# Kernel tuning notes

Hardware: AMD Instinct MI355X
Metric: run time of the kernel (lower is better)

Reference implementation:

```python
import jax, jax.numpy as jnp
import numpy as np
import math

B, S, D, H, HD, P = 2, 2048, 2048, 16, 128, 10
ROPE_BASE = 10000.0


def _rope_tables(seq_len, head_dim):
    inv_freq = 1.0 / (ROPE_BASE ** (np.arange(0, head_dim, 2, dtype=np.float32) / head_dim))
    t = np.arange(seq_len, dtype=np.float32)
    freqs = np.outer(t, inv_freq)                  # [S, hd/2]
    emb = np.concatenate([freqs, freqs], axis=-1)  # [S, hd]
    return jnp.asarray(np.cos(emb)), jnp.asarray(np.sin(emb))


def _rotate_half(x):
    half = x.shape[-1] // 2
    return jnp.concatenate([-x[..., half:], x[..., :half]], axis=-1)


def setup_inputs() -> dict:
    key = jax.random.key(0)
    ks = jax.random.split(key, 8)
    hidden_states = jax.random.normal(ks[0], (B, S, D), dtype=jnp.float32)
    # causal additive mask, llama convention: 0 where allowed, large negative above diagonal
    causal = jnp.triu(jnp.full((S, S), -1e9, dtype=jnp.float32), k=1)
    attention_mask = jnp.broadcast_to(causal[None, None], (B, 1, S, S))
    position_ids = jnp.broadcast_to(jnp.arange(S, dtype=jnp.int64)[None], (B, S))
    scale = 1.0 / math.sqrt(D)
    Wq = jax.random.normal(ks[1], (D, D), dtype=jnp.float32) * scale
    Wk = jax.random.normal(ks[2], (D, D), dtype=jnp.float32) * scale
    Wv = jax.random.normal(ks[3], (D, D), dtype=jnp.float32) * scale
    Wo = jax.random.normal(ks[4], (D, D), dtype=jnp.float32) * scale
    adapter_query = jax.random.normal(ks[5], (P, D), dtype=jnp.float32)
    adapter_gate = jax.random.normal(ks[6], (1, H, 1, 1), dtype=jnp.float32) * 0.1
    return dict(hidden_states=hidden_states, attention_mask=attention_mask,
                position_ids=position_ids, Wq=Wq, Wk=Wk, Wv=Wv, Wo=Wo,
                adapter_query=adapter_query, adapter_gate=adapter_gate)


def reference(hidden_states, attention_mask, position_ids, Wq, Wk, Wv, Wo,
              adapter_query, adapter_gate):
    bsz, q_len, _ = hidden_states.shape
    inv_sqrt_hd = 1.0 / math.sqrt(HD)

    def split_heads(x):  # [B,S,D] -> [B,H,S,hd]
        return x.reshape(bsz, q_len, H, HD).transpose(0, 2, 1, 3)

    q = split_heads(hidden_states @ Wq)
    k = split_heads(hidden_states @ Wk)
    v = split_heads(hidden_states @ Wv)

    # RoPE
    cos_t, sin_t = _rope_tables(q_len, HD)
    cos = cos_t[position_ids][:, None]  # [B,1,S,hd]
    sin = sin_t[position_ids][:, None]
    q = q * cos + _rotate_half(q) * sin
    k = k * cos + _rotate_half(k) * sin

    # main attention
    scores = jnp.einsum('bhqd,bhkd->bhqk', q, k) * inv_sqrt_hd
    scores = scores + attention_mask
    attn = jax.nn.softmax(scores.astype(jnp.float32), axis=-1).astype(q.dtype)
    attn_out = jnp.einsum('bhqk,bhkd->bhqd', attn, v)

    # adapter: soft prompt projected through k/v proj (learn_kv=False), no RoPE
    adapter = jnp.broadcast_to(adapter_query[None], (bsz, P, D))  # [B,P,D]
    a_k = (adapter @ Wk).reshape(bsz, P, H, HD).transpose(0, 2, 1, 3)  # [B,H,P,hd]
    a_v = (adapter @ Wv).reshape(bsz, P, H, HD).transpose(0, 2, 1, 3)
    a_scores = jnp.einsum('bhqd,bhpd->bhqp', q, a_k) * inv_sqrt_hd
    a_w = adapter_gate * jax.nn.softmax(a_scores.astype(jnp.float32), axis=-1).astype(q.dtype)
    a_out = jnp.einsum('bhqp,bhpd->bhqd', a_w, a_v)

    out = attn_out + a_out
    out = out.transpose(0, 2, 1, 3).reshape(bsz, q_len, D)
    return out @ Wo
```

## Files before the change

### kernel.cpp

```cpp
#include <hip/hip_runtime.h>
#include <cstdint>
#include <cstddef>

typedef __bf16 bf16x8 __attribute__((ext_vector_type(8)));
typedef float  f32x4  __attribute__((ext_vector_type(4)));

__device__ __forceinline__ unsigned short f2bf(float f) {
  unsigned int u = __float_as_uint(f);
  u += 0x7FFF + ((u >> 16) & 1);
  return (unsigned short)(u >> 16);
}
__device__ __forceinline__ float bf2f(unsigned short u) {
  return __uint_as_float(((unsigned int)u) << 16);
}

#define SEQ 2048
#define DMODEL 2048
#define NH 16
#define HD 128
#define NB 2
#define NP 10
#define MAUG 4106
#define SCALEL2 (0.08838834764831845f * 1.44269504088896340f)

#define GLOAD_LDS16(g, l) \
  __builtin_amdgcn_global_load_lds((__attribute__((address_space(1))) const void*)(g), \
                                   (__attribute__((address_space(3))) void*)(l), 16, 0, 0)

#define FENCE() asm volatile("" ::: "memory")
#define SBAR() do { FENCE(); __builtin_amdgcn_s_barrier(); FENCE(); } while (0)
#define WAITVM(N) asm volatile("s_waitcnt vmcnt(" #N ")" ::: "memory")

__global__ void k_tables(float* __restrict__ cost, float* __restrict__ sint) {
  int idx = blockIdx.x * 256 + threadIdx.x;
  if (idx >= SEQ * 64) return;
  int s = idx >> 6, i = idx & 63;
  double invf = exp(-((double)(2 * i) / 128.0) * log(10000.0));
  double a = (double)s * invf;
  float c = (float)cos(a), sn = (float)sin(a);
  cost[s * HD + i] = c;  cost[s * HD + 64 + i] = c;
  sint[s * HD + i] = sn; sint[s * HD + 64 + i] = sn;
}

__global__ __launch_bounds__(256) void k_wt(const float* __restrict__ W0,
                                            const float* __restrict__ W1,
                                            const float* __restrict__ W2,
                                            const float* __restrict__ W3,
                                            unsigned short* __restrict__ out) {
  __shared__ float tile[32][33];
  const float* W = (blockIdx.z == 0) ? W0 : (blockIdx.z == 1) ? W1 : (blockIdx.z == 2) ? W2 : W3;
  unsigned short* o = out + (size_t)blockIdx.z * DMODEL * DMODEL;
  int bx = blockIdx.x * 32, by = blockIdx.y * 32;
  int tx = threadIdx.x & 31, ty = threadIdx.x >> 5;
  #pragma unroll
  for (int j = 0; j < 32; j += 8)
    tile[ty + j][tx] = W[(size_t)(bx + ty + j) * DMODEL + by + tx];
  __syncthreads();
  #pragma unroll
  for (int j = 0; j < 32; j += 8)
    o[(size_t)(by + ty + j) * DMODEL + bx + tx] = f2bf(tile[tx][ty + j]);
}

__global__ void k_xaug(const float* __restrict__ X, const float* __restrict__ Aq,
                       unsigned short* __restrict__ xaug) {
  size_t idx = (size_t)blockIdx.x * 256 + threadIdx.x;
  if (idx >= (size_t)MAUG * DMODEL) return;
  size_t row = idx >> 11;
  int col = (int)(idx & 2047);
  float v = (row < (size_t)NB * SEQ) ? X[idx] : Aq[(row - NB * SEQ) * DMODEL + col];
  xaug[idx] = f2bf(v);
}

#define RD_A(dst, bb, MH) do { \
  _Pragma("unroll") for (int i_ = 0; i_ < 4; i_++) \
    _Pragma("unroll") for (int ks_ = 0; ks_ < 2; ks_++) \
      dst[i_][ks_] = *(const bf16x8*)&lds[(bb) + (wr*128 + (MH)*64 + i_*16 + lr)*64 + (((ks_*4+quad) ^ (lr & 7)) * 8)]; \
} while (0)

#define RD_B(dst, bb, NHH) do { \
  _Pragma("unroll") for (int j_ = 0; j_ < 2; j_++) \
    _Pragma("unroll") for (int ks_ = 0; ks_ < 2; ks_++) \
      dst[j_][ks_] = *(const bf16x8*)&lds[(bb) + 16384 + (wc*64 + (NHH)*32 + j_*16 + lr)*64 + (((ks_*4+quad) ^ (lr & 7)) * 8)]; \
} while (0)

#define MM(A, B, MH, NHH) do { \
  __builtin_amdgcn_s_setprio(1); \
  _Pragma("unroll") for (int i_ = 0; i_ < 4; i_++) \
    _Pragma("unroll") for (int j_ = 0; j_ < 2; j_++) { \
      acc[(MH)*4+i_][(NHH)*2+j_] = __builtin_amdgcn_mfma_f32_16x16x32_bf16(A[i_][0], B[j_][0], acc[(MH)*4+i_][(NHH)*2+j_], 0, 0, 0); \
      acc[(MH)*4+i_][(NHH)*2+j_] = __builtin_amdgcn_mfma_f32_16x16x32_bf16(A[i_][1], B[j_][1], acc[(MH)*4+i_][(NHH)*2+j_], 0, 0, 0); \
    } \
  __builtin_amdgcn_s_setprio(0); \
} while (0)

#define STG_AE(nb, ko) do { \
  GLOAD_LDS16(sA + (ko),                      &lds[(nb)*32768 + (qrow)*64 + g8]); \
  GLOAD_LDS16(sA + 128*(size_t)DMODEL + (ko), &lds[(nb)*32768 + (128+qrow)*64 + g8]); } while (0)
#define STG_AO(nb, ko) do { \
  GLOAD_LDS16(sA + 64*(size_t)DMODEL + (ko),  &lds[(nb)*32768 + (64+qrow)*64 + g8]); \
  GLOAD_LDS16(sA + 192*(size_t)DMODEL + (ko), &lds[(nb)*32768 + (192+qrow)*64 + g8]); } while (0)
#define STG_BE(nb, ko) do { \
  GLOAD_LDS16(sB + (ko),                      &lds[(nb)*32768 + 16384 + (qb)*64 + g8]); \
  GLOAD_LDS16(sB + 128*(size_t)DMODEL + (ko), &lds[(nb)*32768 + 16384 + (128+qb)*64 + g8]); } while (0)
#define STG_BO(nb, ko) do { \
  GLOAD_LDS16(sB + 32*(size_t)DMODEL + (ko),  &lds[(nb)*32768 + 16384 + (32+qb)*64 + g8]); \
  GLOAD_LDS16(sB + 160*(size_t)DMODEL + (ko), &lds[(nb)*32768 + 16384 + (160+qb)*64 + g8]); } while (0)

template<int BF16OUT>
__global__ __launch_bounds__(512, 2) void k_gemm256(const unsigned short* __restrict__ A,
                                                    const unsigned short* __restrict__ Bt,
                                                    void* __restrict__ Cv,
                                                    int M, size_t c_stride_mat) {
  __shared__ unsigned short lds[65536];
  const int t = threadIdx.x;
  const int lane = t & 63, w = t >> 6;
  const int lr = lane & 15, quad = lane >> 4;
  const int wr = w >> 2, wc = w & 3;
  const int tm = (M + 255) >> 8;
  const int perz = tm * 8;
  const int qchunk = gridDim.x >> 3;
  const int lin = (blockIdx.x & 7) * qchunk + (blockIdx.x >> 3);
  const int z = lin / perz;
  const int rem = lin - z * perz;
  const int m0 = (rem >> 3) * 256, n0 = (rem & 7) * 256;
  const unsigned short* Bz = Bt + (size_t)z * DMODEL * DMODEL;

  const int qrow = t >> 3;
  const int g8 = (t & 7) * 8;
  const int gsw8 = (((t & 7) ^ (qrow & 7)) * 8);
  const int qb = (qrow < 32) ? qrow : qrow + 32;

  const unsigned short* sA = A + (size_t)(m0 + qrow) * DMODEL + gsw8;
  const unsigned short* sB = Bz + (size_t)(n0 + qb) * DMODEL + gsw8;

  bf16x8 aE[4][2], aO[4][2], bE[2][2], bO[2][2];
  f32x4 acc[8][4];
  #pragma unroll
  for (int i = 0; i < 8; i++)
    #pragma unroll
    for (int j = 0; j < 4; j++) acc[i][j] = (f32x4){0.f, 0.f, 0.f, 0.f};

  STG_AE(0, 0); STG_BE(0, 0); STG_BO(0, 0); STG_AO(0, 0);
  WAITVM(4);
  SBAR();
  RD_A(aE, 0, 0); RD_B(bE, 0, 0);

  for (int kt = 0; kt < DMODEL / 64; kt++) {
    const int base = (kt & 1) << 15;
    const int nb2 = (kt & 1) ^ 1;
    const int nbase = nb2 << 15;
    const int ko = (kt + 1) * 64;
    const bool more = (kt + 1 < DMODEL / 64);

    if (more) { STG_AE(nb2, ko); WAITVM(4); } else WAITVM(2);
    SBAR();
    RD_B(bO, base, 1);
    MM(aE, bE, 0, 0);

    if (more) { STG_BE(nb2, ko); WAITVM(4); } else WAITVM(0);
    SBAR();
    RD_A(aO, base, 1);
    MM(aE, bO, 0, 1);

    if (more) STG_BO(nb2, ko);
    MM(aO, bE, 1, 0);

    if (more) {
      STG_AO(nb2, ko);
      WAITVM(4);
      SBAR();
      RD_A(aE, nbase, 0); RD_B(bE, nbase, 0);
    }
    MM(aO, bO, 1, 1);
  }

  #pragma unroll
  for (int mi = 0; mi < 8; mi++) {
    #pragma unroll
    for (int r = 0; r < 4; r++) {
      int row = m0 + wr * 128 + mi * 16 + quad * 4 + r;
      if (row < M) {
        if (BF16OUT) {
          unsigned short* C = (unsigned short*)Cv + (size_t)z * c_stride_mat;
          #pragma unroll
          for (int n = 0; n < 4; n++)
            C[(size_t)row * DMODEL + n0 + wc * 64 + n * 16 + lr] = f2bf(acc[mi][n][r]);
        } else {
          float* C = (float*)Cv + (size_t)z * c_stride_mat;
          #pragma unroll
          for (int n = 0; n < 4; n++)
            C[(size_t)row * DMODEL + n0 + wc * 64 + n * 16 + lr] = acc[mi][n][r];
        }
      }
    }
  }
}

#define O_RD_A(dst, bb, MH) do { \
  _Pragma("unroll") for (int i_ = 0; i_ < 2; i_++) \
    _Pragma("unroll") for (int ks_ = 0; ks_ < 2; ks_++) \
      dst[i_][ks_] = *(const bf16x8*)&lds[(bb) + (wr*64 + (MH)*32 + i_*16 + lr)*64 + (((ks_*4+quad) ^ (lr & 7)) * 8)]; \
} while (0)

#define O_RD_B(dst, bb, NHH) do { \
  _Pragma("unroll") for (int j_ = 0; j_ < 2; j_++) \
    _Pragma("unroll") for (int ks_ = 0; ks_ < 2; ks_++) \
      dst[j_][ks_] = *(const bf16x8*)&lds[(bb) + 8192 + (wc*64 + (NHH)*32 + j_*16 + lr)*64 + (((ks_*4+quad) ^ (lr & 7)) * 8)]; \
} while (0)

#define O_MM(A, B, MH, NHH) do { \
  __builtin_amdgcn_s_setprio(1); \
  _Pragma("unroll") for (int i_ = 0; i_ < 2; i_++) \
    _Pragma("unroll") for (int j_ = 0; j_ < 2; j_++) { \
      acc[(MH)*2+i_][(NHH)*2+j_] = __builtin_amdgcn_mfma_f32_16x16x32_bf16(A[i_][0], B[j_][0], acc[(MH)*2+i_][(NHH)*2+j_], 0, 0, 0); \
      acc[(MH)*2+i_][(NHH)*2+j_] = __builtin_amdgcn_mfma_f32_16x16x32_bf16(A[i_][1], B[j_][1], acc[(MH)*2+i_][(NHH)*2+j_], 0, 0, 0); \
    } \
  __builtin_amdgcn_s_setprio(0); \
} while (0)

#define O_STG_AE(nb, ko) GLOAD_LDS16(sA + (ko), &lds[(nb)*24576 + (qb)*64 + g8])
#define O_STG_AO(nb, ko) GLOAD_LDS16(sA + 32*(size_t)DMODEL + (ko), &lds[(nb)*24576 + (32+qb)*64 + g8])
#define O_STG_BE(nb, ko) do { \
  GLOAD_LDS16(sB + (ko),                      &lds[(nb)*24576 + 8192 + (qb)*64 + g8]); \
  GLOAD_LDS16(sB + 128*(size_t)DMODEL + (ko), &lds[(nb)*24576 + 8192 + (128+qb)*64 + g8]); } while (0)
#define O_STG_BO(nb, ko) do { \
  GLOAD_LDS16(sB + 32*(size_t)DMODEL + (ko),  &lds[(nb)*24576 + 8192 + (32+qb)*64 + g8]); \
  GLOAD_LDS16(sB + 160*(size_t)DMODEL + (ko), &lds[(nb)*24576 + 8192 + (160+qb)*64 + g8]); } while (0)

__global__ __launch_bounds__(512, 2) void k_gemmo(const unsigned short* __restrict__ A,
                                                  const unsigned short* __restrict__ Bt,
                                                  float* __restrict__ C) {
  __shared__ unsigned short lds[49152];
  const int t = threadIdx.x;
  const int lane = t & 63, w = t >> 6;
  const int lr = lane & 15, quad = lane >> 4;
  const int wr = w >> 2, wc = w & 3;
  const int lin = (blockIdx.x & 7) * 32 + (blockIdx.x >> 3);
  const int m0 = (lin >> 3) * 128, n0 = (lin & 7) * 256;

  const int qrow = t >> 3;
  const int g8 = (t & 7) * 8;
  const int gsw8 = (((t & 7) ^ (qrow & 7)) * 8);
  const int qb = (qrow < 32) ? qrow : qrow + 32;

  const unsigned short* sA = A + (size_t)(m0 + qb) * DMODEL + gsw8;
  const unsigned short* sB = Bt + (size_t)(n0 + qb) * DMODEL + gsw8;

  bf16x8 aE[2][2], aO[2][2], bE[2][2], bO[2][2];
  f32x4 acc[4][4];
  #pragma unroll
  for (int i = 0; i < 4; i++)
    #pragma unroll
    for (int j = 0; j < 4; j++) acc[i][j] = (f32x4){0.f, 0.f, 0.f, 0.f};

  O_STG_AE(0, 0); O_STG_BE(0, 0); O_STG_BO(0, 0); O_STG_AO(0, 0);
  WAITVM(3);
  SBAR();
  O_RD_A(aE, 0, 0); O_RD_B(bE, 0, 0);

  for (int kt = 0; kt < DMODEL / 64; kt++) {
    const int base = (kt & 1) * 24576;
    const int nb2 = (kt & 1) ^ 1;
    const int nbase = nb2 * 24576;
    const int ko = (kt + 1) * 64;
    const bool more = (kt + 1 < DMODEL / 64);

    if (more) { O_STG_AE(nb2, ko); WAITVM(2); } else WAITVM(1);
    SBAR();
    O_RD_B(bO, base, 1);
    O_MM(aE, bE, 0, 0);

    if (more) { O_STG_BE(nb2, ko); WAITVM(3); } else WAITVM(0);
    SBAR();
    O_RD_A(aO, base, 1);
    O_MM(aE, bO, 0, 1);

    if (more) O_STG_BO(nb2, ko);
    O_MM(aO, bE, 1, 0);

    if (more) {
      O_STG_AO(nb2, ko);
      WAITVM(3);
      SBAR();
      O_RD_A(aE, nbase, 0); O_RD_B(bE, nbase, 0);
    }
    O_MM(aO, bO, 1, 1);
  }

  #pragma unroll
  for (int mi = 0; mi < 4; mi++) {
    #pragma unroll
    for (int r = 0; r < 4; r++) {
      int row = m0 + wr * 64 + mi * 16 + quad * 4 + r;
      #pragma unroll
      for (int n = 0; n < 4; n++)
        C[(size_t)row * DMODEL + n0 + wc * 64 + n * 16 + lr] = acc[mi][n][r];
    }
  }
}

__global__ __launch_bounds__(256) void k_rope(const unsigned short* __restrict__ Qf,
                                              const unsigned short* __restrict__ Kf,
                                              const unsigned short* __restrict__ Vf,
                                              const float* __restrict__ cost, const float* __restrict__ sint,
                                              unsigned short* __restrict__ Qb, unsigned short* __restrict__ Kb,
                                              unsigned short* __restrict__ AKb, unsigned short* __restrict__ avt) {
  int row = blockIdx.x;
  int t = threadIdx.x;
  int c0 = t * 8;
  size_t off = (size_t)row * DMODEL + c0;
  if (row < NB * SEQ) {
    int s = row & (SEQ - 1);
    int d0 = c0 & (HD - 1);
    int po = (d0 < 64) ? 64 : -64;
    float sign = (d0 < 64) ? -1.f : 1.f;
    uint4 qv = *(const uint4*)&Qf[off];
    uint4 qp = *(const uint4*)&Qf[off + po];
    uint4 kv = *(const uint4*)&Kf[off];
    uint4 kp = *(const uint4*)&Kf[off + po];
    const unsigned short* qa = (const unsigned short*)&qv;
    const unsigned short* qb2 = (const unsigned short*)&qp;
    const unsigned short* ka = (const unsigned short*)&kv;
    const unsigned short* kb2 = (const unsigned short*)&kp;
    unsigned short oq[8], ok[8];
    #pragma unroll
    for (int j = 0; j < 8; j++) {
      float cv = cost[s * HD + d0 + j], sv = sint[s * HD + d0 + j];
      oq[j] = f2bf(bf2f(qa[j]) * cv + sign * bf2f(qb2[j]) * sv);
      ok[j] = f2bf(bf2f(ka[j]) * cv + sign * bf2f(kb2[j]) * sv);
    }
    *(uint4*)&Qb[off] = *(const uint4*)oq;
    *(uint4*)&Kb[off] = *(const uint4*)ok;
  } else {
    int p = row - NB * SEQ;
    uint4 kv = *(const uint4*)&Kf[off];
    uint4 vv = *(const uint4*)&Vf[off];
    *(uint4*)&AKb[(size_t)p * DMODEL + c0] = kv;
    const unsigned short* vp = (const unsigned short*)&vv;
    #pragma unroll
    for (int j = 0; j < 8; j++)
      avt[(size_t)(c0 + j) * 32 + p] = vp[j];
  }
}

__global__ __launch_bounds__(256) void k_vt(const unsigned short* __restrict__ Vf,
                                            unsigned short* __restrict__ Vt) {
  __shared__ unsigned short tile[64][72];
  const int t = threadIdx.x;
  int s0 = blockIdx.x * 64;
  int d0 = blockIdx.y * 64;
  int b = blockIdx.z >> 4, h = blockIdx.z & 15;
  #pragma unroll
  for (int j = t; j < 512; j += 256) {
    int row = j >> 3, ch = j & 7;
    *(uint4*)&tile[row][ch * 8] =
      *(const uint4*)&Vf[(size_t)(b * SEQ + s0 + row) * DMODEL + h * HD + d0 + ch * 8];
  }
  __syncthreads();
  #pragma unroll
  for (int j = t; j < 512; j += 256) {
    int dr = j >> 3, ch = j & 7;
    unsigned short tmp[8];
    #pragma unroll
    for (int k = 0; k < 8; k++) tmp[k] = tile[ch * 8 + k][dr];
    *(uint4*)&Vt[((size_t)((b * NH + h) * HD + d0 + dr)) * SEQ + s0 + ch * 8] = *(const uint4*)tmp;
  }
}

#define PSTR 68

__global__ __launch_bounds__(256, 3) void k_flash(const unsigned short* __restrict__ Qb,
                                               const unsigned short* __restrict__ Kb,
                                               const unsigned short* __restrict__ Vt,
                                               const unsigned short* __restrict__ AKb,
                                               const unsigned short* __restrict__ avt,
                                               const float* __restrict__ gate,
                                               unsigned short* __restrict__ Obuf,
                                               float* __restrict__ ml,
                                               unsigned short* __restrict__ Aout) {
  const int L = blockIdx.x;
  const int h = L & 15;
  const int slot = 39 - (L >> 4);
  const int b = blockIdx.y;
  int qt, j, P;
  if (slot < 4)       { qt = slot;               j = 0;          P = 1; }
  else if (slot < 12) { int s = slot - 4;  qt = 4 + (s >> 1);  j = s & 1; P = 2; }
  else if (slot < 24) { int s = slot - 12; qt = 8 + s / 3;     j = s % 3; P = 3; }
  else                { int s = slot - 24; qt = 12 + (s >> 2); j = s & 3; P = 4; }

  const int t = threadIdx.x, w = t >> 6, lane = t & 63;
  const int lr = lane & 15, quad = lane >> 4;

  __shared__ unsigned short Ks[64 * 128];
  __shared__ unsigned short Vs[128 * 64];
  __shared__ unsigned short Ps[4][32 * PSTR];
  unsigned short* Ps16 = &Ps[w][0];

  const int row_base = qt * 128 + w * 32;

  bf16x8 qf[2][4];
  #pragma unroll
  for (int mt = 0; mt < 2; mt++)
    #pragma unroll
    for (int kk = 0; kk < 4; kk++)
      qf[mt][kk] = *(const bf16x8*)&Qb[((size_t)(b * SEQ + row_base + mt * 16 + lr)) * DMODEL
                                       + h * HD + kk * 32 + quad * 8];

  f32x4 o[2][8];
  #pragma unroll
  for (int mt = 0; mt < 2; mt++)
    #pragma unroll
    for (int nt = 0; nt < 8; nt++) o[mt][nt] = (f32x4){0.f, 0.f, 0.f, 0.f};
  float l_i[2][4];
  #pragma unroll
  for (int mt = 0; mt < 2; mt++)
    #pragma unroll
    for (int r = 0; r < 4; r++) l_i[mt][r] = 0.f;

  const int krow = t >> 4;
  const int vd = t >> 3, vc = (t & 7) ^ (vd & 7);
  const int ktend = 2 * qt + 2;

  for (int kt = j; kt < ktend; kt += P) {
    __syncthreads();
    #pragma unroll
    for (int jj = 0; jj < 4; jj++) {
      int row = krow + jj * 16;
      int c = (t & 15) ^ (row & 15);
      GLOAD_LDS16(&Kb[((size_t)(b * SEQ + kt * 64 + row)) * DMODEL + h * HD + c * 8],
                  &Ks[(t + jj * 256) * 8]);
    }
    #pragma unroll
    for (int jj = 0; jj < 4; jj++) {
      int d = vd + jj * 32;
      GLOAD_LDS16(&Vt[((size_t)((b * NH + h) * HD + d)) * SEQ + kt * 64 + vc * 8],
                  &Vs[(t + jj * 256) * 8]);
    }
    __syncthreads();

    f32x4 s4[2][4];
    #pragma unroll
    for (int mt = 0; mt < 2; mt++)
      #pragma unroll
      for (int nt = 0; nt < 4; nt++) s4[mt][nt] = (f32x4){0.f, 0.f, 0.f, 0.f};
    #pragma unroll
    for (int nt = 0; nt < 4; nt++)
      #pragma unroll
      for (int kk = 0; kk < 4; kk++) {
        bf16x8 bv = *(const bf16x8*)&Ks[((nt * 16 + lr) * 16 + ((kk * 4 + quad) ^ lr)) * 8];
        s4[0][nt] = __builtin_amdgcn_mfma_f32_16x16x32_bf16(qf[0][kk], bv, s4[0][nt], 0, 0, 0);
        s4[1][nt] = __builtin_amdgcn_mfma_f32_16x16x32_bf16(qf[1][kk], bv, s4[1][nt], 0, 0, 0);
      }

    const int maybe_mask = (kt * 64 + 63 > row_base);
    #pragma unroll
    for (int mt = 0; mt < 2; mt++) {
      #pragma unroll
      for (int nt = 0; nt < 4; nt++) s4[mt][nt] = s4[mt][nt] * SCALEL2;
      if (maybe_mask) {
        #pragma unroll
        for (int nt = 0; nt < 4; nt++) {
          int col = kt * 64 + nt * 16 + lr;
          #pragma unroll
          for (int r = 0; r < 4; r++)
            if (col > row_base + mt * 16 + quad * 4 + r) s4[mt][nt][r] = -__builtin_inff();
        }
      }
      #pragma unroll
      for (int nt = 0; nt < 4; nt++)
        #pragma unroll
        for (int r = 0; r < 4; r++) {
          float p = __builtin_amdgcn_exp2f(s4[mt][nt][r]);
          l_i[mt][r] += p;
          Ps[w][(mt * 16 + quad * 4 + r) * PSTR + nt * 16 + lr] = f2bf(p);
        }
    }
    #pragma unroll
    for (int kk2 = 0; kk2 < 2; kk2++) {
      bf16x8 af0 = *(const bf16x8*)&Ps[w][(lr) * PSTR + kk2 * 32 + quad * 8];
      bf16x8 af1 = *(const bf16x8*)&Ps[w][(16 + lr) * PSTR + kk2 * 32 + quad * 8];
      #pragma unroll
      for (int nt = 0; nt < 8; nt++) {
        bf16x8 bv = *(const bf16x8*)&Vs[((nt * 16 + lr) * 8 + ((kk2 * 4 + quad) ^ (lr & 7))) * 8];
        o[0][nt] = __builtin_amdgcn_mfma_f32_16x16x32_bf16(af0, bv, o[0][nt], 0, 0, 0);
        o[1][nt] = __builtin_amdgcn_mfma_f32_16x16x32_bf16(af1, bv, o[1][nt], 0, 0, 0);
      }
    }
  }

  #pragma unroll
  for (int mt = 0; mt < 2; mt++)
    #pragma unroll
    for (int r = 0; r < 4; r++) {
      float l = l_i[mt][r];
      #pragma unroll
      for (int off = 1; off < 16; off <<= 1) l += __shfl_xor(l, off, 64);
      l_i[mt][r] = l;
    }

  const size_t slotg = (size_t)(b * 16 + h) * 40 + slot;

  if (j == 0) {
    const float g = gate[h];
    #pragma unroll
    for (int mt = 0; mt < 2; mt++) {
      f32x4 as4 = (f32x4){0.f, 0.f, 0.f, 0.f};
      #pragma unroll
      for (int kk = 0; kk < 4; kk++) {
        bf16x8 akf = *(const bf16x8*)&AKb[(size_t)lr * DMODEL + h * HD + kk * 32 + quad * 8];
        as4 = __builtin_amdgcn_mfma_f32_16x16x32_bf16(qf[mt][kk], akf, as4, 0, 0, 0);
      }
      as4 = as4 * SCALEL2;
      float al[4];
      #pragma unroll
      for (int r = 0; r < 4; r++) {
        float p = (lr < NP) ? __builtin_amdgcn_exp2f(as4[r]) : 0.f;
        as4[r] = p;
        float sum = p;
        #pragma unroll
        for (int off = 1; off < 16; off <<= 1) sum += __shfl_xor(sum, off, 64);
        al[r] = sum;
      }
      #pragma unroll
      for (int r = 0; r < 4; r++) {
        Ps[w][(mt * 16 + quad * 4 + r) * PSTR + lr] = f2bf(as4[r]);
        Ps[w][(mt * 16 + quad * 4 + r) * PSTR + 16 + lr] = 0;
      }
      bf16x8 af = *(const bf16x8*)&Ps[w][(mt * 16 + lr) * PSTR + quad * 8];
      f32x4 pa[8];
      #pragma unroll
      for (int nt = 0; nt < 8; nt++) {
        bf16x8 bv = *(const bf16x8*)&avt[(size_t)(h * HD + nt * 16 + lr) * 32 + quad * 8];
        pa[nt] = __builtin_amdgcn_mfma_f32_16x16x32_bf16(af, bv, (f32x4){0.f, 0.f, 0.f, 0.f}, 0, 0, 0);
      }
      float invla[4];
      #pragma unroll
      for (int r = 0; r < 4; r++) invla[r] = g / al[r];
      #pragma unroll
      for (int nt = 0; nt < 8; nt++)
        #pragma unroll
        for (int r = 0; r < 4; r++)
          Ps16[(quad * 4 + r) * 128 + nt * 16 + lr] = f2bf(pa[nt][r] * invla[r]);
      size_t gb = (((size_t)(b * 16 + h) * 16 + qt)) * 16384 + (size_t)(w * 32 + mt * 16) * 128;
      #pragma unroll
      for (int it = 0; it < 4; it++) {
        int i = lane + it * 64;
        int rr = i >> 4, ch = i & 15;
        *(uint4*)&Aout[gb + rr * 128 + ch * 8] = *(const uint4*)&Ps16[rr * 128 + ch * 8];
      }
    }
  }

  #pragma unroll
  for (int mt = 0; mt < 2; mt++) {
    if (lr == 0) {
      #pragma unroll
      for (int r = 0; r < 4; r++) {
        int rl = w * 32 + mt * 16 + quad * 4 + r;
        ml[slotg * 128 + rl] = l_i[mt][r];
      }
    }
    #pragma unroll
    for (int nt = 0; nt < 8; nt++)
      #pragma unroll
      for (int r = 0; r < 4; r++)
        Ps16[(quad * 4 + r) * 128 + nt * 16 + lr] = f2bf(o[mt][nt][r]);
    size_t gb = slotg * 16384 + (size_t)(w * 32 + mt * 16) * 128;
    #pragma unroll
    for (int it = 0; it < 4; it++) {
      int i = lane + it * 64;
      int rr = i >> 4, ch = i & 15;
      *(uint4*)&Obuf[gb + rr * 128 + ch * 8] = *(const uint4*)&Ps16[rr * 128 + ch * 8];
    }
  }
}

__global__ __launch_bounds__(256) void k_merge(const unsigned short* __restrict__ Obuf,
                                               const float* __restrict__ ml,
                                               const unsigned short* __restrict__ Aout,
                                               unsigned short* __restrict__ ab) {
  int idx = blockIdx.x * 256 + threadIdx.x;
  int ch = idx & 15;
  int row = (idx >> 4) & 2047;
  int h = (idx >> 15) & 15;
  int b = idx >> 19;
  int qt = row >> 7, rl = row & 127;
  int start = qt < 4 ? qt : qt < 8 ? 4 + 2 * (qt - 4) : qt < 12 ? 12 + 3 * (qt - 8) : 24 + 4 * (qt - 12);
  int P = qt < 4 ? 1 : qt < 8 ? 2 : qt < 12 ? 3 : 4;
  size_t sbase = (size_t)(b * 16 + h) * 40 + start;
  float den = 0.f;
  float acc[8] = {0.f, 0.f, 0.f, 0.f, 0.f, 0.f, 0.f, 0.f};
  #pragma unroll
  for (int jp = 0; jp < 4; jp++) {
    if (jp < P) {
      den += ml[(sbase + jp) * 128 + rl];
      uint4 ov = *(const uint4*)&Obuf[(sbase + jp) * 16384 + rl * 128 + ch * 8];
      const unsigned short* pv = (const unsigned short*)&ov;
      #pragma unroll
      for (int k = 0; k < 8; k++) acc[k] += bf2f(pv[k]);
    }
  }
  uint4 av = *(const uint4*)&Aout[(((size_t)(b * 16 + h) * 16 + qt)) * 16384 + rl * 128 + ch * 8];
  const unsigned short* pa = (const unsigned short*)&av;
  float dn = 1.0f / den;
  unsigned short res[8];
  #pragma unroll
  for (int k = 0; k < 8; k++) res[k] = f2bf(acc[k] * dn + bf2f(pa[k]));
  *(uint4*)&ab[((size_t)(b * 2048 + row)) * 2048 + h * 128 + ch * 8] = *(const uint4*)res;
}

extern "C" void kernel_launch(void* const* d_in, const int* in_sizes, int n_in,
                              void* d_out, int out_size, void* d_ws, size_t ws_size,
                              hipStream_t stream) {
  const float* hidden = (const float*)d_in[0];
  const float* Wq = (const float*)d_in[3];
  const float* Wk = (const float*)d_in[4];
  const float* Wv = (const float*)d_in[5];
  const float* Wo = (const float*)d_in[6];
  const float* Aq = (const float*)d_in[7];
  const float* gate = (const float*)d_in[8];
  float* out = (float*)d_out;

  char* ws = (char*)d_ws;
  size_t off = 0;
  auto alloc = [&](size_t bytes) -> void* {
    void* p = ws + off;
    off = (off + bytes + 255) & ~(size_t)255;
    return p;
  };
  unsigned short* wt   = (unsigned short*)alloc((size_t)4 * DMODEL * DMODEL * 2);
  unsigned short* xaug = (unsigned short*)alloc((size_t)MAUG * DMODEL * 2);
  unsigned short* qkvb = (unsigned short*)alloc((size_t)3 * MAUG * DMODEL * 2);
  unsigned short* qf = qkvb;
  unsigned short* kf = qkvb + (size_t)MAUG * DMODEL;
  unsigned short* vf = kf + (size_t)MAUG * DMODEL;
  unsigned short* qb  = (unsigned short*)alloc((size_t)NB * SEQ * DMODEL * 2);
  unsigned short* kb  = (unsigned short*)alloc((size_t)NB * SEQ * DMODEL * 2);
  unsigned short* vt  = (unsigned short*)alloc((size_t)NB * SEQ * DMODEL * 2);
  unsigned short* akb = (unsigned short*)alloc((size_t)16 * DMODEL * 2);
  unsigned short* avt = (unsigned short*)alloc((size_t)DMODEL * 32 * 2);
  float* cost = (float*)alloc((size_t)SEQ * HD * 4);
  float* sint = (float*)alloc((size_t)SEQ * HD * 4);
  unsigned short* obuf = (unsigned short*)alloc((size_t)NB * NH * 40 * 16384 * 2);
  float* mlb = (float*)alloc((size_t)NB * NH * 40 * 128 * 4);
  unsigned short* aout = (unsigned short*)alloc((size_t)NB * NH * 16 * 16384 * 2);
  unsigned short* ab = qf;

  k_tables<<<SEQ * 64 / 256, 256, 0, stream>>>(cost, sint);
  k_wt<<<dim3(64, 64, 4), 256, 0, stream>>>(Wq, Wk, Wv, Wo, wt);
  {
    size_t n = (size_t)MAUG * DMODEL;
    k_xaug<<<(unsigned)((n + 255) / 256), 256, 0, stream>>>(hidden, Aq, xaug);
  }
  k_gemm256<1><<<dim3(408), 512, 0, stream>>>(xaug, wt, qkvb, MAUG, (size_t)MAUG * DMODEL);
  hipMemsetAsync(avt, 0, (size_t)DMODEL * 32 * 2, stream);
  k_rope<<<MAUG, 256, 0, stream>>>(qf, kf, vf, cost, sint, qb, kb, akb, avt);
  k_vt<<<dim3(32, 2, 32), 256, 0, stream>>>(vf, vt);
  k_flash<<<dim3(640, 2), 256, 0, stream>>>(qb, kb, vt, akb, avt, gate, obuf, mlb, aout);
  k_merge<<<4096, 256, 0, stream>>>(obuf, mlb, aout, ab);
  k_gemmo<<<dim3(256), 512, 0, stream>>>(ab, wt + (size_t)3 * DMODEL * DMODEL, out);
}
```

Before: 466.8 us.

## Restructure output GEMM pipeline, fold adapter-V zeroing into rope, relax flash occupancy

```diff
diff --git a/kernel.cpp b/kernel.cpp
--- a/kernel.cpp
+++ b/kernel.cpp
@@ -119,7 +119,7 @@
   const int tm = (M + 255) >> 8;
   const int perz = tm * 8;
   const int qchunk = gridDim.x >> 3;
-  const int lin = (blockIdx.x & 7) * qchunk + (blockIdx.x >> 3);
+  const int lin = ((int)blockIdx.x & 7) * qchunk + ((int)blockIdx.x >> 3);
   const int z = lin / perz;
   const int rem = lin - z * perz;
   const int m0 = (rem >> 3) * 256, n0 = (rem & 7) * 256;
@@ -196,24 +196,24 @@
   }
 }
 
-#define O_RD_A(dst, bb, MH) do { \
+#define O_LDA(MH) do { \
   _Pragma("unroll") for (int i_ = 0; i_ < 2; i_++) \
     _Pragma("unroll") for (int ks_ = 0; ks_ < 2; ks_++) \
-      dst[i_][ks_] = *(const bf16x8*)&lds[(bb) + (wr*64 + (MH)*32 + i_*16 + lr)*64 + (((ks_*4+quad) ^ (lr & 7)) * 8)]; \
+      a[i_][ks_] = *(const bf16x8*)&lds[base + (wr*64 + ((MH)*2+i_)*16 + lr)*64 + (((ks_*4+quad) ^ (lr & 7)) * 8)]; \
 } while (0)
 
-#define O_RD_B(dst, bb, NHH) do { \
+#define O_LDB(NHH) do { \
   _Pragma("unroll") for (int j_ = 0; j_ < 2; j_++) \
     _Pragma("unroll") for (int ks_ = 0; ks_ < 2; ks_++) \
-      dst[j_][ks_] = *(const bf16x8*)&lds[(bb) + 8192 + (wc*64 + (NHH)*32 + j_*16 + lr)*64 + (((ks_*4+quad) ^ (lr & 7)) * 8)]; \
+      b[(NHH)*2+j_][ks_] = *(const bf16x8*)&lds[base + 8192 + (wc*64 + ((NHH)*2+j_)*16 + lr)*64 + (((ks_*4+quad) ^ (lr & 7)) * 8)]; \
 } while (0)
 
-#define O_MM(A, B, MH, NHH) do { \
+#define O_MFMA(MH, NHH) do { \
   __builtin_amdgcn_s_setprio(1); \
   _Pragma("unroll") for (int i_ = 0; i_ < 2; i_++) \
     _Pragma("unroll") for (int j_ = 0; j_ < 2; j_++) { \
-      acc[(MH)*2+i_][(NHH)*2+j_] = __builtin_amdgcn_mfma_f32_16x16x32_bf16(A[i_][0], B[j_][0], acc[(MH)*2+i_][(NHH)*2+j_], 0, 0, 0); \
-      acc[(MH)*2+i_][(NHH)*2+j_] = __builtin_amdgcn_mfma_f32_16x16x32_bf16(A[i_][1], B[j_][1], acc[(MH)*2+i_][(NHH)*2+j_], 0, 0, 0); \
+      acc[(MH)*2+i_][(NHH)*2+j_] = __builtin_amdgcn_mfma_f32_16x16x32_bf16(a[i_][0], b[(NHH)*2+j_][0], acc[(MH)*2+i_][(NHH)*2+j_], 0, 0, 0); \
+      acc[(MH)*2+i_][(NHH)*2+j_] = __builtin_amdgcn_mfma_f32_16x16x32_bf16(a[i_][1], b[(NHH)*2+j_][1], acc[(MH)*2+i_][(NHH)*2+j_], 0, 0, 0); \
     } \
   __builtin_amdgcn_s_setprio(0); \
 } while (0)
@@ -235,7 +235,7 @@
   const int lane = t & 63, w = t >> 6;
   const int lr = lane & 15, quad = lane >> 4;
   const int wr = w >> 2, wc = w & 3;
-  const int lin = (blockIdx.x & 7) * 32 + (blockIdx.x >> 3);
+  const int lin = ((int)blockIdx.x & 7) * 32 + ((int)blockIdx.x >> 3);
   const int m0 = (lin >> 3) * 128, n0 = (lin & 7) * 256;
 
   const int qrow = t >> 3;
@@ -246,7 +246,7 @@
   const unsigned short* sA = A + (size_t)(m0 + qb) * DMODEL + gsw8;
   const unsigned short* sB = Bt + (size_t)(n0 + qb) * DMODEL + gsw8;
 
-  bf16x8 aE[2][2], aO[2][2], bE[2][2], bO[2][2];
+  bf16x8 a[2][2], b[4][2];
   f32x4 acc[4][4];
   #pragma unroll
   for (int i = 0; i < 4; i++)
@@ -256,35 +256,39 @@
   O_STG_AE(0, 0); O_STG_BE(0, 0); O_STG_BO(0, 0); O_STG_AO(0, 0);
   WAITVM(3);
   SBAR();
-  O_RD_A(aE, 0, 0); O_RD_B(bE, 0, 0);
 
   for (int kt = 0; kt < DMODEL / 64; kt++) {
     const int base = (kt & 1) * 24576;
-    const int nb2 = (kt & 1) ^ 1;
-    const int nbase = nb2 * 24576;
+    const int nb = (kt & 1) ^ 1;
     const int ko = (kt + 1) * 64;
     const bool more = (kt + 1 < DMODEL / 64);
 
-    if (more) { O_STG_AE(nb2, ko); WAITVM(2); } else WAITVM(1);
-    SBAR();
-    O_RD_B(bO, base, 1);
-    O_MM(aE, bE, 0, 0);
-
-    if (more) { O_STG_BE(nb2, ko); WAITVM(3); } else WAITVM(0);
-    SBAR();
-    O_RD_A(aO, base, 1);
-    O_MM(aE, bO, 0, 1);
-
-    if (more) O_STG_BO(nb2, ko);
-    O_MM(aO, bE, 1, 0);
-
-    if (more) {
-      O_STG_AO(nb2, ko);
-      WAITVM(3);
-      SBAR();
-      O_RD_A(aE, nbase, 0); O_RD_B(bE, nbase, 0);
-    }
-    O_MM(aO, bO, 1, 1);
+    O_LDA(0);
+    O_LDB(0);
+    if (more) O_STG_AE(nb, ko);
+    SBAR();
+    O_MFMA(0, 0);
+    if (more) WAITVM(2); else WAITVM(1);
+    SBAR();
+
+    O_LDB(1);
+    if (more) O_STG_BE(nb, ko);
+    SBAR();
+    O_MFMA(0, 1);
+    if (more) WAITVM(3); else WAITVM(0);
+    SBAR();
+
+    O_LDA(1);
+    if (more) O_STG_BO(nb, ko);
+    SBAR();
+    O_MFMA(1, 0);
+    SBAR();
+
+    if (more) O_STG_AO(nb, ko);
+    SBAR();
+    O_MFMA(1, 1);
+    if (more) WAITVM(3);
+    SBAR();
   }
 
   #pragma unroll
@@ -340,6 +344,12 @@
     #pragma unroll
     for (int j = 0; j < 8; j++)
       avt[(size_t)(c0 + j) * 32 + p] = vp[j];
+    if (p == 0) {
+      #pragma unroll
+      for (int j = 0; j < 8; j++)
+        for (int pp = NP; pp < 32; pp++)
+          avt[(size_t)(c0 + j) * 32 + pp] = 0;
+    }
   }
 }
 
@@ -369,7 +379,7 @@
 
 #define PSTR 68
 
-__global__ __launch_bounds__(256, 3) void k_flash(const unsigned short* __restrict__ Qb,
+__global__ __launch_bounds__(256, 2) void k_flash(const unsigned short* __restrict__ Qb,
                                                const unsigned short* __restrict__ Kb,
                                                const unsigned short* __restrict__ Vt,
                                                const unsigned short* __restrict__ AKb,
@@ -653,7 +663,6 @@
     k_xaug<<<(unsigned)((n + 255) / 256), 256, 0, stream>>>(hidden, Aq, xaug);
   }
   k_gemm256<1><<<dim3(408), 512, 0, stream>>>(xaug, wt, qkvb, MAUG, (size_t)MAUG * DMODEL);
-  hipMemsetAsync(avt, 0, (size_t)DMODEL * 32 * 2, stream);
   k_rope<<<MAUG, 256, 0, stream>>>(qf, kf, vf, cost, sint, qb, kb, akb, avt);
   k_vt<<<dim3(32, 2, 32), 256, 0, stream>>>(vf, vt);
   k_flash<<<dim3(640, 2), 256, 0, stream>>>(qb, kb, vt, akb, avt, gate, obuf, mlb, aout);
```

Result: faster. 420.1 us (-10.0%).
